# Kernel optimization log

Measured on AMD Instinct MI355X. Metric: run time of the kernel, lower is better.

The kernel has to match this reference:

```python
import jax, jax.numpy as jnp
import numpy as np

B, D, H, W, C = 2, 8, 64, 64, 128
NH = 8
WS = (2, 8, 8)
SS = (1, 4, 4)
HEAD_DIM = C // NH
SCALE = HEAD_DIM ** -0.5
MLP_HIDDEN = 4 * C


def _window_partition(x, ws):
    # x: (B, D, H, W, C) -> (B*nW, ws0*ws1*ws2, C)
    b, d, h, w, c = x.shape
    x = x.reshape(b, d // ws[0], ws[0], h // ws[1], ws[1], w // ws[2], ws[2], c)
    return x.transpose(0, 1, 3, 5, 2, 4, 6, 7).reshape(-1, ws[0] * ws[1] * ws[2], c)


def _window_reverse(win, ws, b, d, h, w):
    x = win.reshape(b, d // ws[0], h // ws[1], w // ws[2], ws[0], ws[1], ws[2], -1)
    return x.transpose(0, 1, 4, 2, 5, 3, 6, 7).reshape(b, d, h, w, -1)


def _rel_pos_index(ws):
    coords = np.stack(np.meshgrid(np.arange(ws[0]), np.arange(ws[1]), np.arange(ws[2]), indexing='ij'))
    cf = coords.reshape(3, -1)                       # (3, N)
    rel = (cf[:, :, None] - cf[:, None, :]).transpose(1, 2, 0)  # (N, N, 3)
    rel[:, :, 0] += ws[0] - 1
    rel[:, :, 1] += ws[1] - 1
    rel[:, :, 2] += ws[2] - 1
    rel[:, :, 0] *= (2 * ws[1] - 1) * (2 * ws[2] - 1)
    rel[:, :, 1] *= 2 * ws[2] - 1
    return rel.sum(-1)                               # (N, N)


def _attn_mask(d, h, w, ws, ss):
    img = np.zeros((1, d, h, w, 1), np.float32)
    cnt = 0
    for sd in (slice(-ws[0]), slice(-ws[0], -ss[0]), slice(-ss[0], None)):
        for sh in (slice(-ws[1]), slice(-ws[1], -ss[1]), slice(-ss[1], None)):
            for sw in (slice(-ws[2]), slice(-ws[2], -ss[2]), slice(-ss[2], None)):
                img[:, sd, sh, sw, :] = cnt
                cnt += 1
    mw = _window_partition(img, ws)[..., 0]          # (nW, N)
    am = mw[:, None, :] - mw[:, :, None]             # (nW, N, N)
    return np.where(am != 0, -100.0, 0.0).astype(np.float32)


def _ln(x, g, b):
    m = x.mean(-1, keepdims=True)
    v = ((x - m) ** 2).mean(-1, keepdims=True)
    return (x - m) / jnp.sqrt(v + 1e-5) * g + b


def setup_inputs() -> dict:
    key = jax.random.key(0)
    ks = jax.random.split(key, 8)
    n_bias = (2 * WS[0] - 1) * (2 * WS[1] - 1) * (2 * WS[2] - 1)
    return {
        'x': jax.random.normal(ks[0], (B, D, H, W, C), jnp.float32),
        'qkv_w': jax.random.normal(ks[1], (3 * C, C), jnp.float32) * 0.02,
        'qkv_b': jnp.zeros((3 * C,), jnp.float32),
        'proj_w': jax.random.normal(ks[2], (C, C), jnp.float32) * 0.02,
        'proj_b': jnp.zeros((C,), jnp.float32),
        'rpb': jax.random.normal(ks[3], (n_bias, NH), jnp.float32) * 0.02,
        'ln1_g': jnp.ones((C,), jnp.float32),
        'ln1_b': jnp.zeros((C,), jnp.float32),
        'ln2_g': jnp.ones((C,), jnp.float32),
        'ln2_b': jnp.zeros((C,), jnp.float32),
        'fc1_w': jax.random.normal(ks[4], (MLP_HIDDEN, C), jnp.float32) * 0.02,
        'fc1_b': jnp.zeros((MLP_HIDDEN,), jnp.float32),
        'fc2_w': jax.random.normal(ks[5], (C, MLP_HIDDEN), jnp.float32) * 0.02,
        'fc2_b': jnp.zeros((C,), jnp.float32),
    }


def reference(x, qkv_w, qkv_b, proj_w, proj_b, rpb, ln1_g, ln1_b, ln2_g, ln2_b, fc1_w, fc1_b, fc2_w, fc2_b):
    shortcut = x
    xn = _ln(x, ln1_g, ln1_b)
    # cyclic shift (SW-MSA)
    xs = jnp.roll(xn, (-SS[0], -SS[1], -SS[2]), axis=(1, 2, 3))
    win = _window_partition(xs, WS)                  # (Bw, N, C)
    Bw, N, _ = win.shape
    qkv = (win @ qkv_w.T + qkv_b).reshape(Bw, N, 3, NH, HEAD_DIM).transpose(2, 0, 3, 1, 4)
    q, k, v = qkv[0] * SCALE, qkv[1], qkv[2]         # (Bw, NH, N, d)
    attn = jnp.einsum('bhnd,bhmd->bhnm', q, k)       # (Bw, NH, N, N)
    rpi = _rel_pos_index(WS)
    bias = rpb[rpi.reshape(-1)].reshape(N, N, NH).transpose(2, 0, 1)  # (NH, N, N)
    attn = attn + bias[None]
    mask = jnp.asarray(_attn_mask(D, H, W, WS, SS))  # (nW, N, N)
    nW = mask.shape[0]
    attn = attn.reshape(B, nW, NH, N, N) + mask[None, :, None]
    attn = jax.nn.softmax(attn, axis=-1).reshape(Bw, NH, N, N)
    out = jnp.einsum('bhnm,bhmd->bhnd', attn, v).transpose(0, 2, 1, 3).reshape(Bw, N, C)
    out = out @ proj_w.T + proj_b
    xr = _window_reverse(out, WS, B, D, H, W)
    xr = jnp.roll(xr, SS, axis=(1, 2, 3))
    x1 = shortcut + xr
    # MLP block
    y = _ln(x1, ln2_g, ln2_b)
    y = jax.nn.gelu(y @ fc1_w.T + fc1_b, approximate=False)
    y = y @ fc2_w.T + fc2_b
    return x1 + y
```

## Files before the change

### kernel.cpp

```cpp
#include <hip/hip_runtime.h>
#include <math.h>

typedef short s16x8 __attribute__((ext_vector_type(8)));
typedef short s16x4 __attribute__((ext_vector_type(4)));
typedef float f32x4 __attribute__((ext_vector_type(4)));

#define MFMA(a, b, c)    __builtin_amdgcn_mfma_f32_16x16x32_bf16(a, b, c, 0, 0, 0)
#define MFMA16(a, b, c)  __builtin_amdgcn_mfma_f32_16x16x16bf16_1k(a, b, c, 0, 0, 0)

__device__ __forceinline__ float b2f(ushort u) {
    union { unsigned int i; float f; } v; v.i = ((unsigned int)u) << 16; return v.f;
}
__device__ __forceinline__ ushort f2b(float f) {
    union { float f; unsigned int i; } v; v.f = f;
    unsigned int r = v.i + 0x7fffu + ((v.i >> 16) & 1u);
    return (ushort)(r >> 16);
}
__device__ __forceinline__ float gelu_tanh(float v) {
    float u = 0.7978845608f * (v + 0.044715f * v * v * v);
    float e = __expf(-2.f * fabsf(u));
    float t = (1.f - e) / (1.f + e);
    t = (u < 0.f) ? -t : t;
    return 0.5f * v * (1.f + t);
}

__global__ __launch_bounds__(256) void k0_prep(
    const float* __restrict__ qkv_w, const float* __restrict__ proj_w,
    const float* __restrict__ fc1_w, const float* __restrict__ fc2_w,
    const float* __restrict__ rpb, ushort* __restrict__ wq,
    ushort* __restrict__ wp, ushort* __restrict__ wf, ushort* __restrict__ bm)
{
    int bid = blockIdx.x, tid = threadIdx.x;
    if (bid < 192) { int idx = bid * 256 + tid; wq[idx] = f2b(qkv_w[idx]); return; }
    if (bid < 256) { int idx = (bid - 192) * 256 + tid; wp[idx] = f2b(proj_w[idx]); return; }
    if (bid < 768) {
        int idx = (bid - 256) * 256 + tid;
        wf[idx] = f2b(idx < 65536 ? fc1_w[idx] : fc2_w[idx - 65536]);
        return;
    }
    int bi = bid - 768;
    int cls = bi >> 3, head = bi & 7;
    int ed = (cls >> 2) & 1, eh = (cls >> 1) & 1, ew = cls & 1;
    int j = tid & 127;
    int tdj = j >> 6, thj = (j >> 3) & 7, twj = j & 7;
    int regj = (ed ? (tdj + 1) : 0) * 9
             + (eh ? ((thj < 4) ? 1 : 2) : 0) * 3
             + (ew ? ((twj < 4) ? 1 : 2) : 0);
    ushort* bmp = bm + (long)bi * 16384;
    for (int ii = 0; ii < 64; ++ii) {
        int i = (tid >> 7) * 64 + ii;
        int tdi = i >> 6, thi = (i >> 3) & 7, twi = i & 7;
        int regi = (ed ? (tdi + 1) : 0) * 9
                 + (eh ? ((thi < 4) ? 1 : 2) : 0) * 3
                 + (ew ? ((twi < 4) ? 1 : 2) : 0);
        int rpi = (tdi - tdj + 1) * 225 + (thi - thj + 7) * 15 + (twi - twj + 7);
        float v = rpb[rpi * 8 + head] + ((regi != regj) ? -100.f : 0.f);
        bmp[i * 128 + j] = f2b(v);
    }
}

__global__ __launch_bounds__(256) void k23(
    const float* __restrict__ x, const float* __restrict__ g,
    const float* __restrict__ be, const ushort* __restrict__ wq,
    const float* __restrict__ qkv_b, const ushort* __restrict__ bm,
    ushort* __restrict__ obuf)
{
    __shared__ __align__(16) ushort As[128][136];
    __shared__ __align__(16) ushort qb[128][132];
    __shared__ __align__(16) ushort kb[128][132];
    int tid = threadIdx.x;
    int wi = blockIdx.x;
    int wd = (wi >> 6) & 3, wh = (wi >> 3) & 7, ww = wi & 7;
    int cls = ((wd == 3) << 2) | ((wh == 7) << 1) | (ww == 7);
    {
        int row = tid >> 1, half = tid & 1;
        int b = wi >> 8;
        int td = row >> 6, th = (row >> 3) & 7, tw = row & 7;
        int d = (wd * 2 + td + 1) & 7;
        int h = (wh * 8 + th + 4) & 63;
        int w = (ww * 8 + tw + 4) & 63;
        long src = (((long)((b * 8 + d) * 64 + h)) * 64 + w) * 128 + half * 64;
        float vals[64];
        float s = 0.f, q = 0.f;
        #pragma unroll
        for (int i = 0; i < 16; ++i) {
            float4 u = *(const float4*)&x[src + i * 4];
            vals[i * 4 + 0] = u.x; vals[i * 4 + 1] = u.y;
            vals[i * 4 + 2] = u.z; vals[i * 4 + 3] = u.w;
            s += u.x + u.y + u.z + u.w;
            q += u.x * u.x + u.y * u.y + u.z * u.z + u.w * u.w;
        }
        s += __shfl_xor(s, 1);
        q += __shfl_xor(q, 1);
        float mean = s * (1.f / 128.f);
        float rstd = rsqrtf(q * (1.f / 128.f) - mean * mean + 1e-5f);
        #pragma unroll
        for (int i = 0; i < 8; ++i) {
            ushort pk[8];
            #pragma unroll
            for (int jj = 0; jj < 8; ++jj) {
                int c = half * 64 + i * 8 + jj;
                pk[jj] = f2b((vals[i * 8 + jj] - mean) * rstd * g[c] + be[c]);
            }
            *(uint4*)&As[row][half * 64 + i * 8] = *(uint4*)pk;
        }
    }
    __syncthreads();
    int wv = tid >> 6, lane = tid & 63, li = lane & 15, quad = lane >> 4;
    int wm = wv >> 1, wn = wv & 1;
    for (int nb = 0; nb < 3; ++nb) {
        f32x4 acc[4][4] = {};
        for (int s = 0; s < 4; ++s) {
            s16x8 a[4], bw[4];
            #pragma unroll
            for (int mi = 0; mi < 4; ++mi)
                a[mi] = *(const s16x8*)&As[wm * 64 + mi * 16 + li][s * 32 + quad * 8];
            #pragma unroll
            for (int ni = 0; ni < 4; ++ni)
                bw[ni] = *(const s16x8*)&wq[(long)(nb * 128 + wn * 64 + ni * 16 + li) * 128
                                            + s * 32 + quad * 8];
            #pragma unroll
            for (int mi = 0; mi < 4; ++mi)
                #pragma unroll
                for (int ni = 0; ni < 4; ++ni)
                    acc[mi][ni] = MFMA(a[mi], bw[ni], acc[mi][ni]);
        }
        if (nb == 2) __syncthreads();
        #pragma unroll
        for (int mi = 0; mi < 4; ++mi)
            #pragma unroll
            for (int ni = 0; ni < 4; ++ni) {
                int gcol = nb * 128 + wn * 64 + ni * 16 + li;
                float bias = qkv_b[gcol];
                float scale = (nb == 0) ? 0.25f : 1.f;
                #pragma unroll
                for (int r = 0; r < 4; ++r) {
                    int trow = wm * 64 + mi * 16 + quad * 4 + r;
                    ushort val = f2b((acc[mi][ni][r] + bias) * scale);
                    if (nb == 0) {
                        qb[trow][gcol] = val;
                    } else if (nb == 1) {
                        kb[trow][gcol - 128] = val;
                    } else {
                        int c2 = gcol - 256, hh = c2 >> 4, dd = c2 & 15;
                        ((ushort*)As)[hh * 2176 + dd * 136 + trow] = val;
                    }
                }
            }
    }
    __syncthreads();
    const ushort* vtp = (const ushort*)As;
    for (int hh2 = 0; hh2 < 2; ++hh2) {
        int h = wv * 2 + hh2;
        long bmb = (long)(cls * 8 + h) * 16384;
        long ob = (long)wi * 16384 + h * 2048;
        for (int qq = 0; qq < 4; ++qq) {
            int row0 = qq * 32;
            s16x4 qf0 = *(const s16x4*)&qb[row0 + li][h * 16 + quad * 4];
            s16x4 qf1 = *(const s16x4*)&qb[row0 + 16 + li][h * 16 + quad * 4];
            float ps0 = 0.f, ps1 = 0.f;
            uint pa0[8][2], pa1[8][2];
            #pragma unroll
            for (int mi = 0; mi < 8; ++mi) {
                s16x4 kf = *(const s16x4*)&kb[mi * 16 + li][h * 16 + quad * 4];
                f32x4 z = {0.f, 0.f, 0.f, 0.f};
                f32x4 s0 = MFMA16(kf, qf0, z);
                f32x4 s1 = MFMA16(kf, qf1, z);
                s16x4 b0 = *(const s16x4*)&bm[bmb + (row0 + li) * 128 + mi * 16 + quad * 4];
                s16x4 b1 = *(const s16x4*)&bm[bmb + (row0 + 16 + li) * 128 + mi * 16 + quad * 4];
                float e0 = __expf(s0[0] + b2f((ushort)b0[0]));
                float e1 = __expf(s0[1] + b2f((ushort)b0[1]));
                float e2 = __expf(s0[2] + b2f((ushort)b0[2]));
                float e3 = __expf(s0[3] + b2f((ushort)b0[3]));
                ps0 += (e0 + e1) + (e2 + e3);
                pa0[mi][0] = (uint)f2b(e0) | ((uint)f2b(e1) << 16);
                pa0[mi][1] = (uint)f2b(e2) | ((uint)f2b(e3) << 16);
                float f0 = __expf(s1[0] + b2f((ushort)b1[0]));
                float f1 = __expf(s1[1] + b2f((ushort)b1[1]));
                float f2 = __expf(s1[2] + b2f((ushort)b1[2]));
                float f3 = __expf(s1[3] + b2f((ushort)b1[3]));
                ps1 += (f0 + f1) + (f2 + f3);
                pa1[mi][0] = (uint)f2b(f0) | ((uint)f2b(f1) << 16);
                pa1[mi][1] = (uint)f2b(f2) | ((uint)f2b(f3) << 16);
            }
            ps0 += __shfl_xor(ps0, 16); ps0 += __shfl_xor(ps0, 32);
            ps1 += __shfl_xor(ps1, 16); ps1 += __shfl_xor(ps1, 32);
            float inv0 = 1.f / ps0, inv1 = 1.f / ps1;
            f32x4 pc0 = {0.f, 0.f, 0.f, 0.f}, pc1 = {0.f, 0.f, 0.f, 0.f};
            #pragma unroll
            for (int mi = 0; mi < 8; ++mi) {
                s16x4 vf = *(const s16x4*)&vtp[h * 2176 + li * 136 + mi * 16 + quad * 4];
                union { uint2 u; s16x4 v; } a0, a1;
                a0.u.x = pa0[mi][0]; a0.u.y = pa0[mi][1];
                a1.u.x = pa1[mi][0]; a1.u.y = pa1[mi][1];
                pc0 = MFMA16(a0.v, vf, pc0);
                pc1 = MFMA16(a1.v, vf, pc1);
            }
            #pragma unroll
            for (int r = 0; r < 4; ++r) {
                float oi0 = __shfl(inv0, quad * 4 + r);
                float oi1 = __shfl(inv1, quad * 4 + r);
                int i0 = row0 + quad * 4 + r;
                int i1 = row0 + 16 + quad * 4 + r;
                obuf[ob + (long)i0 * 16 + li] = f2b(pc0[r] * oi0);
                obuf[ob + (long)i1 * 16 + li] = f2b(pc1[r] * oi1);
            }
        }
    }
}

__global__ __launch_bounds__(256) void k45(
    const ushort* __restrict__ ao, const ushort* __restrict__ wp,
    const float* __restrict__ proj_b, const float* __restrict__ x,
    const float* __restrict__ g2, const float* __restrict__ be2,
    const ushort* __restrict__ wf1, const float* __restrict__ fc1_b,
    const ushort* __restrict__ wf2, const float* __restrict__ fc2_b,
    float* __restrict__ out)
{
    __shared__ __align__(16) ushort As[64][132];
    __shared__ __align__(16) ushort x1t[64][132];
    __shared__ __align__(16) ushort hs[64][132];
    __shared__ float redS[4][64];
    __shared__ float redQ[4][64];
    int tid = threadIdx.x;
    int b = blockIdx.x;
    int wi = b >> 1, half64 = b & 1;
    int wd = (wi >> 6) & 3, wh = (wi >> 3) & 7, ww = wi & 7;
    int bb = wi >> 8;
    long aob = (long)wi * 16384;
    int tok0 = half64 * 64;
    #pragma unroll
    for (int i = 0; i < 4; ++i) {
        int slot = tid + i * 256;
        int row = slot & 63, hsl = slot >> 6;
        *(uint4*)&As[row][hsl * 8] =
            *(const uint4*)&ao[aob + (hsl >> 1) * 2048 + (long)(tok0 + row) * 16 + (hsl & 1) * 8];
    }
    __syncthreads();
    int wv = tid >> 6, lane = tid & 63, li = lane & 15, quad = lane >> 4;
    int wm = wv >> 1, wn = wv & 1;
    f32x4 acc[2][4] = {};
    for (int s = 0; s < 4; ++s) {
        s16x8 a[2], bw[4];
        #pragma unroll
        for (int mi = 0; mi < 2; ++mi)
            a[mi] = *(const s16x8*)&As[wm * 32 + mi * 16 + li][s * 32 + quad * 8];
        #pragma unroll
        for (int ni = 0; ni < 4; ++ni)
            bw[ni] = *(const s16x8*)&wp[(long)(wn * 64 + ni * 16 + li) * 128 + s * 32 + quad * 8];
        #pragma unroll
        for (int mi = 0; mi < 2; ++mi)
            #pragma unroll
            for (int ni = 0; ni < 4; ++ni)
                acc[mi][ni] = MFMA(a[mi], bw[ni], acc[mi][ni]);
    }
    #pragma unroll
    for (int mi = 0; mi < 2; ++mi) {
        #pragma unroll
        for (int r = 0; r < 4; ++r) {
            int lrow = wm * 32 + mi * 16 + quad * 4 + r;
            int t = half64 * 64 + lrow;
            int td = t >> 6, th = (t >> 3) & 7, tw = t & 7;
            int d = (wd * 2 + td + 1) & 7, h = (wh * 8 + th + 4) & 63, w = (ww * 8 + tw + 4) & 63;
            long di = (((long)((bb * 8 + d) * 64 + h)) * 64 + w) * 128;
            #pragma unroll
            for (int ni = 0; ni < 4; ++ni) {
                int col = wn * 64 + ni * 16 + li;
                x1t[lrow][col] = f2b(acc[mi][ni][r] + proj_b[col] + x[di + col]);
            }
        }
    }
    __syncthreads();
    {
        int token = tid & 63, part = tid >> 6;
        float vals[32];
        float s = 0.f, q = 0.f;
        #pragma unroll
        for (int i = 0; i < 4; ++i) {
            uint4 u = *(const uint4*)&x1t[token][part * 32 + i * 8];
            const ushort* p = (const ushort*)&u;
            #pragma unroll
            for (int j = 0; j < 8; ++j) { float f = b2f(p[j]); vals[i * 8 + j] = f; s += f; q += f * f; }
        }
        redS[part][token] = s; redQ[part][token] = q;
        __syncthreads();
        float st = 0.f, qt = 0.f;
        #pragma unroll
        for (int p2 = 0; p2 < 4; ++p2) { st += redS[p2][token]; qt += redQ[p2][token]; }
        float mean = st * (1.f / 128.f);
        float rstd = rsqrtf(qt * (1.f / 128.f) - mean * mean + 1e-5f);
        #pragma unroll
        for (int i = 0; i < 4; ++i) {
            ushort packed[8];
            #pragma unroll
            for (int j = 0; j < 8; ++j) {
                int c = part * 32 + i * 8 + j;
                packed[j] = f2b((vals[i * 8 + j] - mean) * rstd * g2[c] + be2[c]);
            }
            *(uint4*)&As[token][part * 32 + i * 8] = *(uint4*)packed;
        }
    }
    __syncthreads();
    f32x4 yacc[2][4] = {};
    for (int hc = 0; hc < 4; ++hc) {
        f32x4 hacc[2][4] = {};
        #pragma unroll
        for (int kk = 0; kk < 4; ++kk) {
            s16x8 a[2], bw[4];
            #pragma unroll
            for (int mi = 0; mi < 2; ++mi)
                a[mi] = *(const s16x8*)&As[wm * 32 + mi * 16 + li][kk * 32 + quad * 8];
            #pragma unroll
            for (int ni = 0; ni < 4; ++ni)
                bw[ni] = *(const s16x8*)&wf1[(long)(hc * 128 + wn * 64 + ni * 16 + li) * 128
                                             + kk * 32 + quad * 8];
            #pragma unroll
            for (int mi = 0; mi < 2; ++mi)
                #pragma unroll
                for (int ni = 0; ni < 4; ++ni)
                    hacc[mi][ni] = MFMA(a[mi], bw[ni], hacc[mi][ni]);
        }
        #pragma unroll
        for (int mi = 0; mi < 2; ++mi)
            #pragma unroll
            for (int ni = 0; ni < 4; ++ni) {
                int col = wn * 64 + ni * 16 + li;
                float bbv = fc1_b[hc * 128 + col];
                #pragma unroll
                for (int r = 0; r < 4; ++r) {
                    int row = wm * 32 + mi * 16 + quad * 4 + r;
                    hs[row][col] = f2b(gelu_tanh(hacc[mi][ni][r] + bbv));
                }
            }
        __syncthreads();
        #pragma unroll
        for (int kk = 0; kk < 4; ++kk) {
            s16x8 a[2], bw[4];
            #pragma unroll
            for (int mi = 0; mi < 2; ++mi)
                a[mi] = *(const s16x8*)&hs[wm * 32 + mi * 16 + li][kk * 32 + quad * 8];
            #pragma unroll
            for (int ni = 0; ni < 4; ++ni)
                bw[ni] = *(const s16x8*)&wf2[(long)(wn * 64 + ni * 16 + li) * 512
                                             + hc * 128 + kk * 32 + quad * 8];
            #pragma unroll
            for (int mi = 0; mi < 2; ++mi)
                #pragma unroll
                for (int ni = 0; ni < 4; ++ni)
                    yacc[mi][ni] = MFMA(a[mi], bw[ni], yacc[mi][ni]);
        }
        __syncthreads();
    }
    #pragma unroll
    for (int mi = 0; mi < 2; ++mi) {
        #pragma unroll
        for (int r = 0; r < 4; ++r) {
            int lrow = wm * 32 + mi * 16 + quad * 4 + r;
            int t = half64 * 64 + lrow;
            int td = t >> 6, th = (t >> 3) & 7, tw = t & 7;
            int d = (wd * 2 + td + 1) & 7, h = (wh * 8 + th + 4) & 63, w = (ww * 8 + tw + 4) & 63;
            long di = (((long)((bb * 8 + d) * 64 + h)) * 64 + w) * 128;
            #pragma unroll
            for (int ni = 0; ni < 4; ++ni) {
                int col = wn * 64 + ni * 16 + li;
                out[di + col] = b2f(x1t[lrow][col]) + yacc[mi][ni][r] + fc2_b[col];
            }
        }
    }
}

extern "C" void kernel_launch(void* const* d_in, const int* in_sizes, int n_in,
                              void* d_out, int out_size, void* d_ws, size_t ws_size,
                              hipStream_t stream)
{
    (void)in_sizes; (void)n_in; (void)out_size; (void)ws_size;
    const float* x      = (const float*)d_in[0];
    const float* qkv_w  = (const float*)d_in[1];
    const float* qkv_b  = (const float*)d_in[2];
    const float* proj_w = (const float*)d_in[3];
    const float* proj_b = (const float*)d_in[4];
    const float* rpb    = (const float*)d_in[5];
    const float* ln1_g  = (const float*)d_in[6];
    const float* ln1_b  = (const float*)d_in[7];
    const float* ln2_g  = (const float*)d_in[8];
    const float* ln2_b  = (const float*)d_in[9];
    const float* fc1_w  = (const float*)d_in[10];
    const float* fc1_b  = (const float*)d_in[11];
    const float* fc2_w  = (const float*)d_in[12];
    const float* fc2_b  = (const float*)d_in[13];
    float* out = (float*)d_out;

    ushort* obuf = (ushort*)d_ws;
    ushort* wq   = (ushort*)((char*)d_ws + 50331648);
    ushort* wp   = wq + 49152;
    ushort* wf   = wp + 16384;
    ushort* bm   = wf + 131072;

    hipLaunchKernelGGL(k0_prep, dim3(832), dim3(256), 0, stream,
                       qkv_w, proj_w, fc1_w, fc2_w, rpb, wq, wp, wf, bm);
    hipLaunchKernelGGL(k23, dim3(512), dim3(256), 0, stream,
                       x, ln1_g, ln1_b, wq, qkv_b, bm, obuf);
    hipLaunchKernelGGL(k45, dim3(1024), dim3(256), 0, stream,
                       obuf, wp, proj_b, x, ln2_g, ln2_b,
                       wf, fc1_b, wf + 65536, fc2_b, out);
}
```

Baseline: 269.6 us.

## Split attention kernel across two blocks per window by head halves

The fused LN+QKV+attention kernel now launches two blocks per window, each computing Q/K/V and attention for four of the eight heads. Shared Q/K buffers shrink to half width and each wave handles one head instead of two. This doubles the grid to fill more CUs and cuts LDS use per block. The cost is that LayerNorm and the window load are done twice per window. The workspace offset for the weights also moves down.

```diff
diff --git a/kernel.cpp b/kernel.cpp
--- a/kernel.cpp
+++ b/kernel.cpp
@@ -66,10 +66,10 @@
     ushort* __restrict__ obuf)
 {
     __shared__ __align__(16) ushort As[128][136];
-    __shared__ __align__(16) ushort qb[128][132];
-    __shared__ __align__(16) ushort kb[128][132];
+    __shared__ __align__(16) ushort qb[128][68];
+    __shared__ __align__(16) ushort kb[128][68];
     int tid = threadIdx.x;
-    int wi = blockIdx.x;
+    int wi = blockIdx.x >> 1, hh = blockIdx.x & 1;
     int wd = (wi >> 6) & 3, wh = (wi >> 3) & 7, ww = wi & 7;
     int cls = ((wd == 3) << 2) | ((wh == 7) << 1) | (ww == 7);
     {
@@ -109,28 +109,29 @@
     int wv = tid >> 6, lane = tid & 63, li = lane & 15, quad = lane >> 4;
     int wm = wv >> 1, wn = wv & 1;
     for (int nb = 0; nb < 3; ++nb) {
-        f32x4 acc[4][4] = {};
+        f32x4 acc[4][2] = {};
         for (int s = 0; s < 4; ++s) {
-            s16x8 a[4], bw[4];
+            s16x8 a[4], bw[2];
             #pragma unroll
             for (int mi = 0; mi < 4; ++mi)
                 a[mi] = *(const s16x8*)&As[wm * 64 + mi * 16 + li][s * 32 + quad * 8];
             #pragma unroll
-            for (int ni = 0; ni < 4; ++ni)
-                bw[ni] = *(const s16x8*)&wq[(long)(nb * 128 + wn * 64 + ni * 16 + li) * 128
+            for (int ni = 0; ni < 2; ++ni)
+                bw[ni] = *(const s16x8*)&wq[(long)(nb * 128 + hh * 64 + wn * 32 + ni * 16 + li) * 128
                                             + s * 32 + quad * 8];
             #pragma unroll
             for (int mi = 0; mi < 4; ++mi)
                 #pragma unroll
-                for (int ni = 0; ni < 4; ++ni)
+                for (int ni = 0; ni < 2; ++ni)
                     acc[mi][ni] = MFMA(a[mi], bw[ni], acc[mi][ni]);
         }
         if (nb == 2) __syncthreads();
         #pragma unroll
         for (int mi = 0; mi < 4; ++mi)
             #pragma unroll
-            for (int ni = 0; ni < 4; ++ni) {
-                int gcol = nb * 128 + wn * 64 + ni * 16 + li;
+            for (int ni = 0; ni < 2; ++ni) {
+                int lcol = wn * 32 + ni * 16 + li;
+                int gcol = nb * 128 + hh * 64 + lcol;
                 float bias = qkv_b[gcol];
                 float scale = (nb == 0) ? 0.25f : 1.f;
                 #pragma unroll
@@ -138,31 +139,31 @@
                     int trow = wm * 64 + mi * 16 + quad * 4 + r;
                     ushort val = f2b((acc[mi][ni][r] + bias) * scale);
                     if (nb == 0) {
-                        qb[trow][gcol] = val;
+                        qb[trow][lcol] = val;
                     } else if (nb == 1) {
-                        kb[trow][gcol - 128] = val;
+                        kb[trow][lcol] = val;
                     } else {
-                        int c2 = gcol - 256, hh = c2 >> 4, dd = c2 & 15;
-                        ((ushort*)As)[hh * 2176 + dd * 136 + trow] = val;
+                        int hl = lcol >> 4, dd = lcol & 15;
+                        ((ushort*)As)[hl * 2176 + dd * 136 + trow] = val;
                     }
                 }
             }
     }
     __syncthreads();
     const ushort* vtp = (const ushort*)As;
-    for (int hh2 = 0; hh2 < 2; ++hh2) {
-        int h = wv * 2 + hh2;
-        long bmb = (long)(cls * 8 + h) * 16384;
-        long ob = (long)wi * 16384 + h * 2048;
+    {
+        int hl = wv, hg = hh * 4 + wv;
+        long bmb = (long)(cls * 8 + hg) * 16384;
+        long ob = (long)wi * 16384 + hg * 2048;
         for (int qq = 0; qq < 4; ++qq) {
             int row0 = qq * 32;
-            s16x4 qf0 = *(const s16x4*)&qb[row0 + li][h * 16 + quad * 4];
-            s16x4 qf1 = *(const s16x4*)&qb[row0 + 16 + li][h * 16 + quad * 4];
+            s16x4 qf0 = *(const s16x4*)&qb[row0 + li][hl * 16 + quad * 4];
+            s16x4 qf1 = *(const s16x4*)&qb[row0 + 16 + li][hl * 16 + quad * 4];
             float ps0 = 0.f, ps1 = 0.f;
             uint pa0[8][2], pa1[8][2];
             #pragma unroll
             for (int mi = 0; mi < 8; ++mi) {
-                s16x4 kf = *(const s16x4*)&kb[mi * 16 + li][h * 16 + quad * 4];
+                s16x4 kf = *(const s16x4*)&kb[mi * 16 + li][hl * 16 + quad * 4];
                 f32x4 z = {0.f, 0.f, 0.f, 0.f};
                 f32x4 s0 = MFMA16(kf, qf0, z);
                 f32x4 s1 = MFMA16(kf, qf1, z);
@@ -189,7 +190,7 @@
             f32x4 pc0 = {0.f, 0.f, 0.f, 0.f}, pc1 = {0.f, 0.f, 0.f, 0.f};
             #pragma unroll
             for (int mi = 0; mi < 8; ++mi) {
-                s16x4 vf = *(const s16x4*)&vtp[h * 2176 + li * 136 + mi * 16 + quad * 4];
+                s16x4 vf = *(const s16x4*)&vtp[hl * 2176 + li * 136 + mi * 16 + quad * 4];
                 union { uint2 u; s16x4 v; } a0, a1;
                 a0.u.x = pa0[mi][0]; a0.u.y = pa0[mi][1];
                 a1.u.x = pa1[mi][0]; a1.u.y = pa1[mi][1];
@@ -391,14 +392,14 @@
     float* out = (float*)d_out;
 
     ushort* obuf = (ushort*)d_ws;
-    ushort* wq   = (ushort*)((char*)d_ws + 50331648);
+    ushort* wq   = (ushort*)((char*)d_ws + 16777216);
     ushort* wp   = wq + 49152;
     ushort* wf   = wp + 16384;
     ushort* bm   = wf + 131072;
 
     hipLaunchKernelGGL(k0_prep, dim3(832), dim3(256), 0, stream,
                        qkv_w, proj_w, fc1_w, fc2_w, rpb, wq, wp, wf, bm);
-    hipLaunchKernelGGL(k23, dim3(512), dim3(256), 0, stream,
+    hipLaunchKernelGGL(k23, dim3(1024), dim3(256), 0, stream,
                        x, ln1_g, ln1_b, wq, qkv_b, bm, obuf);
     hipLaunchKernelGGL(k45, dim3(1024), dim3(256), 0, stream,
                        obuf, wp, proj_b, x, ln2_g, ln2_b,
```

After: 267.5 us. About the same (-0.8%).
